# Kernel optimization log

Measured on AMD Instinct MI355X. Metric: run time of the kernel, lower is better.

The kernel has to match this reference:

```python
import jax, jax.numpy as jnp
import numpy as np
from jax import lax


def setup_inputs() -> dict:
    key = jax.random.key(0)
    ks = jax.random.split(key, 6)
    B, L, D, H, K = 32, 256, 16, 64, 5
    T = L - K + 1            # 252
    S = (T // 2) * H         # 8064
    return {
        "x": jax.random.normal(ks[0], (B, L, D), dtype=jnp.float32),
        "conv_w": jax.random.normal(ks[1], (D, H, K), dtype=jnp.float32) * 0.1,
        "conv_b": jax.random.normal(ks[2], (D, H), dtype=jnp.float32) * 0.1,
        "deconv_w": jax.random.normal(ks[3], (D, H, K), dtype=jnp.float32) * 0.1,
        "deconv_b": jax.random.normal(ks[4], (D,), dtype=jnp.float32) * 0.1,
        "W_attn": jax.random.normal(ks[5], (S, S), dtype=jnp.float32) * 0.01,
    }


def reference(x, conv_w, conv_b, deconv_w, deconv_b, W_attn):
    B, L, D = x.shape
    _, H, K = conv_w.shape
    T = L - K + 1
    P = T // 2
    S = P * H

    xt = jnp.transpose(x, (0, 2, 1))  # [B, D, L]
    # per-channel Conv1d(1->H) as one grouped conv: kernel [D*H, 1, K], groups=D
    y = lax.conv_general_dilated(
        xt, conv_w.reshape(D * H, 1, K), (1,), "VALID",
        dimension_numbers=("NCH", "OIH", "NCH"), feature_group_count=D,
    ) + conv_b.reshape(1, D * H, 1)
    y = jax.nn.relu(y)  # [B, D*H, T]

    # per-channel ConvTranspose1d(H->1) == full conv with flipped kernel, groups=D
    recon = lax.conv_general_dilated(
        y, deconv_w[..., ::-1], (1,), [(K - 1, K - 1)],
        dimension_numbers=("NCH", "OIH", "NCH"), feature_group_count=D,
    ) + deconv_b.reshape(1, D, 1)  # [B, D, L]

    # AvgPool1d(kernel=2, stride=2) then flatten(H, P) per channel
    pooled = y.reshape(B, D, H, P, 2).mean(axis=-1)  # [B, D, H, P]
    flat = pooled.reshape(B, D, S)                   # [B, D, S]

    main = flat[:, 0]        # [B, S]
    aux = flat[:, 1:]        # [B, D-1, S]

    # 'general' score: main . (aux @ W^T)  ==  (main @ W) . aux
    m = main @ W_attn                              # [B, S]
    scores = jnp.einsum("bt,bdt->bd", m, aux)      # [B, D-1]
    attn = jax.nn.softmax(scores, axis=-1)         # [B, D-1]
    weighted = jnp.einsum("bd,bds->bs", attn, aux)  # [B, S]

    out = jnp.concatenate([main[:, None, :], weighted[:, None, :]], axis=2)  # [B,1,2S]
    return out, attn[:, None, :], recon
```

## Files before the change

### kernel.cpp

```cpp
#include <hip/hip_runtime.h>
#include <math.h>

#define BB 32
#define LL 256
#define DD 16
#define HH 64
#define KK 5
#define TT 252
#define PP 126
#define SS 8064
#define NCHUNK 12
#define CHUNK 672
#define NKT 21

typedef __attribute__((ext_vector_type(8))) short bf16x8;
typedef __attribute__((ext_vector_type(4))) float f32x4;

__device__ __forceinline__ unsigned short f2bf(float f) {
  unsigned int u = __float_as_uint(f);
  u += 0x7FFFu + ((u >> 16) & 1u);
  return (unsigned short)(u >> 16);
}
__device__ __forceinline__ float bf2f(unsigned short h) {
  return __uint_as_float(((unsigned int)h) << 16);
}

__global__ __launch_bounds__(256) void k12_conv_recon(
    const float* __restrict__ x, const float* __restrict__ cw,
    const float* __restrict__ cb, const float* __restrict__ dw,
    const float* __restrict__ db, float* __restrict__ flat,
    unsigned short* __restrict__ mainH, unsigned short* __restrict__ mainL,
    float* __restrict__ recon) {
  __shared__ float ylds[HH * TT];
  __shared__ float xs[LL];
  __shared__ float cws[HH * KK];
  __shared__ float dws[HH * KK];
  __shared__ float cbs[HH];

  int bd = blockIdx.x;
  int b = bd / DD, d = bd % DD;
  int tid = threadIdx.x;

  xs[tid] = x[((size_t)b * LL + tid) * DD + d];
  for (int i = tid; i < HH * KK; i += 256) {
    cws[i] = cw[(size_t)d * HH * KK + i];
    dws[i] = dw[(size_t)d * HH * KK + i];
  }
  if (tid < HH) cbs[tid] = cb[d * HH + tid];
  __syncthreads();

  {
    int h = tid >> 2, a = tid & 3;
    int t0 = a * 63;
    float w0 = cws[h * KK + 0], w1 = cws[h * KK + 1], w2 = cws[h * KK + 2],
          w3 = cws[h * KK + 3], w4 = cws[h * KK + 4];
    float bias = cbs[h];
    float x0 = xs[t0], x1 = xs[t0 + 1], x2 = xs[t0 + 2], x3 = xs[t0 + 3],
          x4 = xs[t0 + 4];
    float* yrow = ylds + h * TT + t0;
    #pragma unroll 7
    for (int t = 0; t < 63; ++t) {
      float yv = fmaf(w4, x4, fmaf(w3, x3, fmaf(w2, x2, fmaf(w1, x1, fmaf(w0, x0, bias)))));
      yrow[t] = fmaxf(yv, 0.f);
      x0 = x1; x1 = x2; x2 = x3; x3 = x4;
      if (t < 62) x4 = xs[t0 + t + 5];
    }
  }
  __syncthreads();

  for (int i = tid; i < HH * PP; i += 256) {
    int h = i / PP, p = i - h * PP;
    float pooled = 0.5f * (ylds[h * TT + 2 * p] + ylds[h * TT + 2 * p + 1]);
    flat[(size_t)bd * SS + i] = pooled;
    if (d == 0) {
      unsigned short hb = f2bf(pooled);
      mainH[(size_t)b * SS + i] = hb;
      mainL[(size_t)b * SS + i] = f2bf(pooled - bf2f(hb));
    }
  }

  {
    int l = tid;
    float acc = db[d];
    for (int h = 0; h < HH; ++h) {
      const float* yl = ylds + h * TT;
      #pragma unroll
      for (int j = 0; j < KK; ++j) {
        int t = l - j;
        if (t >= 0 && t < TT) acc = fmaf(yl[t], dws[h * KK + j], acc);
      }
    }
    recon[(size_t)bd * LL + l] = acc;
  }
}

__global__ __launch_bounds__(256) void k3_mfma(
    const float* __restrict__ W, const unsigned short* __restrict__ mainH,
    const unsigned short* __restrict__ mainL, float* __restrict__ partial) {
  __shared__ unsigned short AH[2][1024];
  __shared__ unsigned short AL[2][1024];
  __shared__ unsigned short BH[2][2048];
  __shared__ unsigned short BL[2][2048];

  int tid = threadIdx.x;
  int chunk = blockIdx.y;
  int s0 = chunk * CHUNK;
  int cbase = blockIdx.x * 64;

  int lane = tid & 63;
  int wv = tid >> 6;
  int mr = wv & 1;
  int nt0 = (wv >> 1) * 2;

  f32x4 acc0 = {0.f, 0.f, 0.f, 0.f};
  f32x4 acc1 = {0.f, 0.f, 0.f, 0.f};

  int sc = tid & 63;
  int sg = tid >> 6;

  int aoff  = (lane >> 4) * 256 + ((lane & 15) + 16 * mr) * 8;
  int b0off = (lane >> 4) * 512 + ((lane & 15) + 16 * nt0) * 8;
  int b1off = b0off + 128;

  const float* wbase = W + (size_t)(s0 + sg * 8) * SS + cbase + sc;
  int ab = tid >> 2, aq = tid & 3;
  size_t abase = (size_t)ab * SS + (size_t)(s0 + aq * 8);

  float f0, f1, f2, f3, f4, f5, f6, f7;
  bf16x8 aHr, aLr;

#define LOADW(KT) {                                                   \
    const float* p_ = wbase + (size_t)(KT) * 32 * SS;                 \
    f0 = p_[0];                f1 = p_[(size_t)SS];                   \
    f2 = p_[2 * (size_t)SS];   f3 = p_[3 * (size_t)SS];               \
    f4 = p_[4 * (size_t)SS];   f5 = p_[5 * (size_t)SS];               \
    f6 = p_[6 * (size_t)SS];   f7 = p_[7 * (size_t)SS]; }

#define LOADA(KT) if (tid < 128) {                                    \
    aHr = *(const bf16x8*)(mainH + abase + (KT) * 32);                \
    aLr = *(const bf16x8*)(mainL + abase + (KT) * 32); }

#define SPLIT1(F, J) {                                                \
    unsigned int u_ = __float_as_uint(F);                             \
    vh[J] = (short)(u_ >> 16);                                        \
    float rem_ = F - __uint_as_float(u_ & 0xFFFF0000u);               \
    vl[J] = (short)(__float_as_uint(rem_) >> 16); }

#define CVTW(BUF) {                                                   \
    bf16x8 vh, vl;                                                    \
    SPLIT1(f0, 0) SPLIT1(f1, 1) SPLIT1(f2, 2) SPLIT1(f3, 3)           \
    SPLIT1(f4, 4) SPLIT1(f5, 5) SPLIT1(f6, 6) SPLIT1(f7, 7)           \
    *(bf16x8*)&BH[BUF][sg * 512 + sc * 8] = vh;                       \
    *(bf16x8*)&BL[BUF][sg * 512 + sc * 8] = vl; }

#define WRITEA(BUF) if (tid < 128) {                                  \
    *(bf16x8*)&AH[BUF][aq * 256 + ab * 8] = aHr;                      \
    *(bf16x8*)&AL[BUF][aq * 256 + ab * 8] = aLr; }

#define DOMFMA(BUF) {                                                 \
    bf16x8 ah  = *(const bf16x8*)&AH[BUF][aoff];                      \
    bf16x8 al  = *(const bf16x8*)&AL[BUF][aoff];                      \
    bf16x8 b0h = *(const bf16x8*)&BH[BUF][b0off];                     \
    bf16x8 b0l = *(const bf16x8*)&BL[BUF][b0off];                     \
    bf16x8 b1h = *(const bf16x8*)&BH[BUF][b1off];                     \
    bf16x8 b1l = *(const bf16x8*)&BL[BUF][b1off];                     \
    acc0 = __builtin_amdgcn_mfma_f32_16x16x32_bf16(ah, b0h, acc0, 0, 0, 0); \
    acc0 = __builtin_amdgcn_mfma_f32_16x16x32_bf16(ah, b0l, acc0, 0, 0, 0); \
    acc0 = __builtin_amdgcn_mfma_f32_16x16x32_bf16(al, b0h, acc0, 0, 0, 0); \
    acc1 = __builtin_amdgcn_mfma_f32_16x16x32_bf16(ah, b1h, acc1, 0, 0, 0); \
    acc1 = __builtin_amdgcn_mfma_f32_16x16x32_bf16(ah, b1l, acc1, 0, 0, 0); \
    acc1 = __builtin_amdgcn_mfma_f32_16x16x32_bf16(al, b1h, acc1, 0, 0, 0); }

  LOADW(0) LOADA(0)
  CVTW(0) WRITEA(0)
  LOADW(1) LOADA(1)
  __syncthreads();

  #pragma unroll 1
  for (int kt = 0; kt < NKT; ++kt) {
    DOMFMA(kt & 1)
    if (kt + 1 < NKT) { CVTW((kt + 1) & 1) WRITEA((kt + 1) & 1) }
    if (kt + 2 < NKT) { LOADW(kt + 2) LOADA(kt + 2) }
    __syncthreads();
  }

  int row0 = mr * 16 + (lane >> 4) * 4;
  int col0 = cbase + nt0 * 16 + (lane & 15);
  float* pp = partial + ((size_t)chunk * BB + row0) * SS + col0;
  pp[0 * (size_t)SS] = acc0[0];
  pp[1 * (size_t)SS] = acc0[1];
  pp[2 * (size_t)SS] = acc0[2];
  pp[3 * (size_t)SS] = acc0[3];
  pp += 16;
  pp[0 * (size_t)SS] = acc1[0];
  pp[1 * (size_t)SS] = acc1[1];
  pp[2 * (size_t)SS] = acc1[2];
  pp[3 * (size_t)SS] = acc1[3];
#undef LOADW
#undef LOADA
#undef SPLIT1
#undef CVTW
#undef WRITEA
#undef DOMFMA
}

__global__ __launch_bounds__(256) void k3b_reduce(
    const float4* __restrict__ partial, float4* __restrict__ m) {
  int i = blockIdx.x * 256 + threadIdx.x;
  float4 s = make_float4(0.f, 0.f, 0.f, 0.f);
  #pragma unroll
  for (int c = 0; c < NCHUNK; ++c) {
    float4 v = partial[(size_t)c * (BB * SS / 4) + i];
    s.x += v.x; s.y += v.y; s.z += v.z; s.w += v.w;
  }
  m[i] = s;
}

__global__ __launch_bounds__(256) void k4_scores(
    const float* __restrict__ m, const float* __restrict__ flat,
    float* __restrict__ scores) {
  int bd = blockIdx.x;
  int b = bd / 15, dd = bd % 15;
  const float* mb = m + (size_t)b * SS;
  const float* ab = flat + ((size_t)b * DD + 1 + dd) * SS;
  float p = 0.f;
  for (int s = threadIdx.x; s < SS; s += 256) p = fmaf(mb[s], ab[s], p);
  #pragma unroll
  for (int o = 32; o; o >>= 1) p += __shfl_xor(p, o);
  __shared__ float red[4];
  if ((threadIdx.x & 63) == 0) red[threadIdx.x >> 6] = p;
  __syncthreads();
  if (threadIdx.x == 0) scores[bd] = red[0] + red[1] + red[2] + red[3];
}

__global__ __launch_bounds__(64) void k5_softmax(
    const float* __restrict__ scores, float* __restrict__ attn_out) {
  int b = blockIdx.x;
  int lane = threadIdx.x;
  float v = (lane < 15) ? scores[b * 15 + lane] : -INFINITY;
  float mx = v;
  #pragma unroll
  for (int o = 32; o; o >>= 1) mx = fmaxf(mx, __shfl_xor(mx, o));
  float e = (lane < 15) ? expf(v - mx) : 0.f;
  float sum = e;
  #pragma unroll
  for (int o = 32; o; o >>= 1) sum += __shfl_xor(sum, o);
  if (lane < 15) attn_out[b * 15 + lane] = e / sum;
}

__global__ __launch_bounds__(256) void k6_out(
    const float* __restrict__ flat, const float* __restrict__ attn,
    float* __restrict__ out) {
  int b = blockIdx.y;
  int s = blockIdx.x * 256 + threadIdx.x;
  if (s >= SS) return;
  const float* fb = flat + (size_t)b * DD * SS;
  out[(size_t)b * 2 * SS + s] = fb[s];
  float w = 0.f;
  #pragma unroll
  for (int d = 0; d < 15; ++d)
    w = fmaf(attn[b * 15 + d], fb[(size_t)(1 + d) * SS + s], w);
  out[(size_t)b * 2 * SS + SS + s] = w;
}

extern "C" void kernel_launch(void* const* d_in, const int* in_sizes, int n_in,
                              void* d_out, int out_size, void* d_ws, size_t ws_size,
                              hipStream_t stream) {
  const float* x        = (const float*)d_in[0];
  const float* conv_w   = (const float*)d_in[1];
  const float* conv_b   = (const float*)d_in[2];
  const float* deconv_w = (const float*)d_in[3];
  const float* deconv_b = (const float*)d_in[4];
  const float* W_attn   = (const float*)d_in[5];
  float* out = (float*)d_out;

  const size_t ATTN_OFF  = (size_t)BB * 2 * SS;
  const size_t RECON_OFF = ATTN_OFF + (size_t)BB * 15;

  float* ws      = (float*)d_ws;
  float* partial = ws;
  float* flat    = partial + (size_t)NCHUNK * BB * SS;
  unsigned short* mainH = (unsigned short*)(flat + (size_t)BB * DD * SS);
  unsigned short* mainL = mainH + (size_t)BB * SS;
  float* m       = (float*)(mainL + (size_t)BB * SS);
  float* scores  = m + (size_t)BB * SS;

  k12_conv_recon<<<dim3(BB * DD), dim3(256), 0, stream>>>(
      x, conv_w, conv_b, deconv_w, deconv_b, flat, mainH, mainL, out + RECON_OFF);

  k3_mfma<<<dim3(SS / 64, NCHUNK), dim3(256), 0, stream>>>(
      W_attn, mainH, mainL, partial);

  k3b_reduce<<<dim3((BB * SS / 4) / 256), dim3(256), 0, stream>>>(
      (const float4*)partial, (float4*)m);

  k4_scores<<<dim3(BB * 15), dim3(256), 0, stream>>>(m, flat, scores);

  k5_softmax<<<dim3(BB), dim3(64), 0, stream>>>(scores, out + ATTN_OFF);

  k6_out<<<dim3((SS + 255) / 256, BB), dim3(256), 0, stream>>>(
      flat, out + ATTN_OFF, out);
}
```

Baseline: 101.0 us.

## Widen GEMV-MFMA column tile to 128 with float2 W loads and split prefetch registers

The k3_mfma kernel now has each block cover 128 output columns instead of 64. Each thread loads float2 pairs of W_attn and each wave computes four 16x16 MFMA tiles instead of two. The main loop is unrolled by two with separate even and odd register sets, so the next global loads are issued before the MFMAs on the current buffer. The aim is fewer blocks, wider memory transactions and better latency hiding on the W stream, at the cost of more registers and LDS per block and half as many blocks in the grid.

```diff
diff --git a/kernel.cpp b/kernel.cpp
--- a/kernel.cpp
+++ b/kernel.cpp
@@ -99,106 +99,133 @@
     const unsigned short* __restrict__ mainL, float* __restrict__ partial) {
   __shared__ unsigned short AH[2][1024];
   __shared__ unsigned short AL[2][1024];
-  __shared__ unsigned short BH[2][2048];
-  __shared__ unsigned short BL[2][2048];
+  __shared__ unsigned short BH[2][4096];
+  __shared__ unsigned short BL[2][4096];
 
   int tid = threadIdx.x;
   int chunk = blockIdx.y;
   int s0 = chunk * CHUNK;
-  int cbase = blockIdx.x * 64;
+  int cbase = blockIdx.x * 128;
 
   int lane = tid & 63;
   int wv = tid >> 6;
   int mr = wv & 1;
-  int nt0 = (wv >> 1) * 2;
-
-  f32x4 acc0 = {0.f, 0.f, 0.f, 0.f};
-  f32x4 acc1 = {0.f, 0.f, 0.f, 0.f};
-
-  int sc = tid & 63;
+  int ctb = (wv >> 1) * 4;
+
+  f32x4 c0 = {0.f, 0.f, 0.f, 0.f};
+  f32x4 c1 = {0.f, 0.f, 0.f, 0.f};
+  f32x4 c2 = {0.f, 0.f, 0.f, 0.f};
+  f32x4 c3 = {0.f, 0.f, 0.f, 0.f};
+
+  int sc2 = (tid & 63) * 2;
   int sg = tid >> 6;
-
-  int aoff  = (lane >> 4) * 256 + ((lane & 15) + 16 * mr) * 8;
-  int b0off = (lane >> 4) * 512 + ((lane & 15) + 16 * nt0) * 8;
-  int b1off = b0off + 128;
-
-  const float* wbase = W + (size_t)(s0 + sg * 8) * SS + cbase + sc;
+  const float* wbase = W + (size_t)(s0 + sg * 8) * SS + cbase + sc2;
+
   int ab = tid >> 2, aq = tid & 3;
   size_t abase = (size_t)ab * SS + (size_t)(s0 + aq * 8);
 
-  float f0, f1, f2, f3, f4, f5, f6, f7;
-  bf16x8 aHr, aLr;
-
-#define LOADW(KT) {                                                   \
+  int aoff  = (lane >> 4) * 256 + ((lane & 15) + 16 * mr) * 8;
+  int boff0 = (lane >> 4) * 1024 + ((ctb) * 16 + (lane & 15)) * 8;
+
+  float2 e0, e1, e2, e3, e4, e5, e6, e7;
+  float2 o0, o1, o2, o3, o4, o5, o6, o7;
+  bf16x8 aEH, aEL, aOH, aOL;
+
+#define LOADW(R0,R1,R2,R3,R4,R5,R6,R7, KT) {                          \
     const float* p_ = wbase + (size_t)(KT) * 32 * SS;                 \
-    f0 = p_[0];                f1 = p_[(size_t)SS];                   \
-    f2 = p_[2 * (size_t)SS];   f3 = p_[3 * (size_t)SS];               \
-    f4 = p_[4 * (size_t)SS];   f5 = p_[5 * (size_t)SS];               \
-    f6 = p_[6 * (size_t)SS];   f7 = p_[7 * (size_t)SS]; }
-
-#define LOADA(KT) if (tid < 128) {                                    \
-    aHr = *(const bf16x8*)(mainH + abase + (KT) * 32);                \
-    aLr = *(const bf16x8*)(mainL + abase + (KT) * 32); }
-
-#define SPLIT1(F, J) {                                                \
-    unsigned int u_ = __float_as_uint(F);                             \
-    vh[J] = (short)(u_ >> 16);                                        \
-    float rem_ = F - __uint_as_float(u_ & 0xFFFF0000u);               \
-    vl[J] = (short)(__float_as_uint(rem_) >> 16); }
-
-#define CVTW(BUF) {                                                   \
-    bf16x8 vh, vl;                                                    \
-    SPLIT1(f0, 0) SPLIT1(f1, 1) SPLIT1(f2, 2) SPLIT1(f3, 3)           \
-    SPLIT1(f4, 4) SPLIT1(f5, 5) SPLIT1(f6, 6) SPLIT1(f7, 7)           \
-    *(bf16x8*)&BH[BUF][sg * 512 + sc * 8] = vh;                       \
-    *(bf16x8*)&BL[BUF][sg * 512 + sc * 8] = vl; }
-
-#define WRITEA(BUF) if (tid < 128) {                                  \
-    *(bf16x8*)&AH[BUF][aq * 256 + ab * 8] = aHr;                      \
-    *(bf16x8*)&AL[BUF][aq * 256 + ab * 8] = aLr; }
+    R0 = *(const float2*)(p_);                                        \
+    R1 = *(const float2*)(p_ + (size_t)SS);                           \
+    R2 = *(const float2*)(p_ + 2 * (size_t)SS);                       \
+    R3 = *(const float2*)(p_ + 3 * (size_t)SS);                       \
+    R4 = *(const float2*)(p_ + 4 * (size_t)SS);                       \
+    R5 = *(const float2*)(p_ + 5 * (size_t)SS);                       \
+    R6 = *(const float2*)(p_ + 6 * (size_t)SS);                       \
+    R7 = *(const float2*)(p_ + 7 * (size_t)SS); }
+
+#define LOADA(RH, RL, KT) if (tid < 128) {                            \
+    RH = *(const bf16x8*)(mainH + abase + (KT) * 32);                 \
+    RL = *(const bf16x8*)(mainL + abase + (KT) * 32); }
+
+#define SPLITC(F, J) {                                                \
+    unsigned int ux_ = __float_as_uint(F.x);                          \
+    unsigned int uy_ = __float_as_uint(F.y);                          \
+    h0[J] = (short)(ux_ >> 16); h1[J] = (short)(uy_ >> 16);           \
+    float rx_ = F.x - __uint_as_float(ux_ & 0xFFFF0000u);             \
+    float ry_ = F.y - __uint_as_float(uy_ & 0xFFFF0000u);             \
+    l0[J] = (short)(__float_as_uint(rx_) >> 16);                      \
+    l1[J] = (short)(__float_as_uint(ry_) >> 16); }
+
+#define CVTW(R0,R1,R2,R3,R4,R5,R6,R7, BUF) {                          \
+    bf16x8 h0, h1, l0, l1;                                            \
+    SPLITC(R0, 0) SPLITC(R1, 1) SPLITC(R2, 2) SPLITC(R3, 3)           \
+    SPLITC(R4, 4) SPLITC(R5, 5) SPLITC(R6, 6) SPLITC(R7, 7)           \
+    *(bf16x8*)&BH[BUF][sg * 1024 + sc2 * 8]     = h0;                 \
+    *(bf16x8*)&BH[BUF][sg * 1024 + sc2 * 8 + 8] = h1;                 \
+    *(bf16x8*)&BL[BUF][sg * 1024 + sc2 * 8]     = l0;                 \
+    *(bf16x8*)&BL[BUF][sg * 1024 + sc2 * 8 + 8] = l1; }
+
+#define WRITEA(RH, RL, BUF) if (tid < 128) {                          \
+    *(bf16x8*)&AH[BUF][aq * 256 + ab * 8] = RH;                       \
+    *(bf16x8*)&AL[BUF][aq * 256 + ab * 8] = RL; }
 
 #define DOMFMA(BUF) {                                                 \
     bf16x8 ah  = *(const bf16x8*)&AH[BUF][aoff];                      \
     bf16x8 al  = *(const bf16x8*)&AL[BUF][aoff];                      \
-    bf16x8 b0h = *(const bf16x8*)&BH[BUF][b0off];                     \
-    bf16x8 b0l = *(const bf16x8*)&BL[BUF][b0off];                     \
-    bf16x8 b1h = *(const bf16x8*)&BH[BUF][b1off];                     \
-    bf16x8 b1l = *(const bf16x8*)&BL[BUF][b1off];                     \
-    acc0 = __builtin_amdgcn_mfma_f32_16x16x32_bf16(ah, b0h, acc0, 0, 0, 0); \
-    acc0 = __builtin_amdgcn_mfma_f32_16x16x32_bf16(ah, b0l, acc0, 0, 0, 0); \
-    acc0 = __builtin_amdgcn_mfma_f32_16x16x32_bf16(al, b0h, acc0, 0, 0, 0); \
-    acc1 = __builtin_amdgcn_mfma_f32_16x16x32_bf16(ah, b1h, acc1, 0, 0, 0); \
-    acc1 = __builtin_amdgcn_mfma_f32_16x16x32_bf16(ah, b1l, acc1, 0, 0, 0); \
-    acc1 = __builtin_amdgcn_mfma_f32_16x16x32_bf16(al, b1h, acc1, 0, 0, 0); }
-
-  LOADW(0) LOADA(0)
-  CVTW(0) WRITEA(0)
-  LOADW(1) LOADA(1)
+    bf16x8 bh0 = *(const bf16x8*)&BH[BUF][boff0];                     \
+    bf16x8 bl0 = *(const bf16x8*)&BL[BUF][boff0];                     \
+    bf16x8 bh1 = *(const bf16x8*)&BH[BUF][boff0 + 128];               \
+    bf16x8 bl1 = *(const bf16x8*)&BL[BUF][boff0 + 128];               \
+    bf16x8 bh2 = *(const bf16x8*)&BH[BUF][boff0 + 256];               \
+    bf16x8 bl2 = *(const bf16x8*)&BL[BUF][boff0 + 256];               \
+    bf16x8 bh3 = *(const bf16x8*)&BH[BUF][boff0 + 384];               \
+    bf16x8 bl3 = *(const bf16x8*)&BL[BUF][boff0 + 384];               \
+    c0 = __builtin_amdgcn_mfma_f32_16x16x32_bf16(ah, bh0, c0, 0, 0, 0); \
+    c0 = __builtin_amdgcn_mfma_f32_16x16x32_bf16(ah, bl0, c0, 0, 0, 0); \
+    c0 = __builtin_amdgcn_mfma_f32_16x16x32_bf16(al, bh0, c0, 0, 0, 0); \
+    c1 = __builtin_amdgcn_mfma_f32_16x16x32_bf16(ah, bh1, c1, 0, 0, 0); \
+    c1 = __builtin_amdgcn_mfma_f32_16x16x32_bf16(ah, bl1, c1, 0, 0, 0); \
+    c1 = __builtin_amdgcn_mfma_f32_16x16x32_bf16(al, bh1, c1, 0, 0, 0); \
+    c2 = __builtin_amdgcn_mfma_f32_16x16x32_bf16(ah, bh2, c2, 0, 0, 0); \
+    c2 = __builtin_amdgcn_mfma_f32_16x16x32_bf16(ah, bl2, c2, 0, 0, 0); \
+    c2 = __builtin_amdgcn_mfma_f32_16x16x32_bf16(al, bh2, c2, 0, 0, 0); \
+    c3 = __builtin_amdgcn_mfma_f32_16x16x32_bf16(ah, bh3, c3, 0, 0, 0); \
+    c3 = __builtin_amdgcn_mfma_f32_16x16x32_bf16(ah, bl3, c3, 0, 0, 0); \
+    c3 = __builtin_amdgcn_mfma_f32_16x16x32_bf16(al, bh3, c3, 0, 0, 0); }
+
+  LOADW(e0,e1,e2,e3,e4,e5,e6,e7, 0) LOADA(aEH, aEL, 0)
+  CVTW(e0,e1,e2,e3,e4,e5,e6,e7, 0) WRITEA(aEH, aEL, 0)
+  LOADW(o0,o1,o2,o3,o4,o5,o6,o7, 1) LOADA(aOH, aOL, 1)
   __syncthreads();
 
   #pragma unroll 1
-  for (int kt = 0; kt < NKT; ++kt) {
-    DOMFMA(kt & 1)
-    if (kt + 1 < NKT) { CVTW((kt + 1) & 1) WRITEA((kt + 1) & 1) }
-    if (kt + 2 < NKT) { LOADW(kt + 2) LOADA(kt + 2) }
+  for (int kt = 0; kt < NKT - 1; kt += 2) {
+    LOADW(e0,e1,e2,e3,e4,e5,e6,e7, kt + 2) LOADA(aEH, aEL, kt + 2)
+    DOMFMA(0)
+    CVTW(o0,o1,o2,o3,o4,o5,o6,o7, 1) WRITEA(aOH, aOL, 1)
     __syncthreads();
-  }
+    if (kt + 3 < NKT) {
+      LOADW(o0,o1,o2,o3,o4,o5,o6,o7, kt + 3) LOADA(aOH, aOL, kt + 3)
+    }
+    DOMFMA(1)
+    CVTW(e0,e1,e2,e3,e4,e5,e6,e7, 0) WRITEA(aEH, aEL, 0)
+    __syncthreads();
+  }
+  DOMFMA(0)
 
   int row0 = mr * 16 + (lane >> 4) * 4;
-  int col0 = cbase + nt0 * 16 + (lane & 15);
+  int col0 = cbase + ctb * 16 + (lane & 15);
   float* pp = partial + ((size_t)chunk * BB + row0) * SS + col0;
-  pp[0 * (size_t)SS] = acc0[0];
-  pp[1 * (size_t)SS] = acc0[1];
-  pp[2 * (size_t)SS] = acc0[2];
-  pp[3 * (size_t)SS] = acc0[3];
-  pp += 16;
-  pp[0 * (size_t)SS] = acc1[0];
-  pp[1 * (size_t)SS] = acc1[1];
-  pp[2 * (size_t)SS] = acc1[2];
-  pp[3 * (size_t)SS] = acc1[3];
+  #pragma unroll
+  for (int r = 0; r < 4; ++r) pp[(size_t)r * SS]      = c0[r];
+  #pragma unroll
+  for (int r = 0; r < 4; ++r) pp[(size_t)r * SS + 16] = c1[r];
+  #pragma unroll
+  for (int r = 0; r < 4; ++r) pp[(size_t)r * SS + 32] = c2[r];
+  #pragma unroll
+  for (int r = 0; r < 4; ++r) pp[(size_t)r * SS + 48] = c3[r];
 #undef LOADW
 #undef LOADA
-#undef SPLIT1
+#undef SPLITC
 #undef CVTW
 #undef WRITEA
 #undef DOMFMA
@@ -288,7 +315,7 @@
   k12_conv_recon<<<dim3(BB * DD), dim3(256), 0, stream>>>(
       x, conv_w, conv_b, deconv_w, deconv_b, flat, mainH, mainL, out + RECON_OFF);
 
-  k3_mfma<<<dim3(SS / 64, NCHUNK), dim3(256), 0, stream>>>(
+  k3_mfma<<<dim3(SS / 128, NCHUNK), dim3(256), 0, stream>>>(
       W_attn, mainH, mainL, partial);
 
   k3b_reduce<<<dim3((BB * SS / 4) / 256), dim3(256), 0, stream>>>(
```

Result: faster. 97.98 us (-3.0%).
